# Kernel optimization log

Measured on AMD Instinct MI355X. Metric: run time of the kernel, lower is better.

## Reference

```python
import jax, jax.numpy as jnp
import numpy as np

N, D, E, H, K = 16384, 1024, 16, 4096, 2


def setup_inputs() -> dict:
    key = jax.random.key(0)
    ks = jax.random.split(key, 6)
    s = 0.02
    return {
        "x": jax.random.normal(ks[0], (N, D), jnp.float32),
        "Wr": jax.random.normal(ks[1], (D, E), jnp.float32) * s,
        "br": jnp.zeros((E,), jnp.float32),
        "Wn": jax.random.normal(ks[2], (D, E), jnp.float32) * s,
        "bn": jnp.zeros((E,), jnp.float32),
        "W1": jax.random.normal(ks[3], (E, D, H), jnp.float32) * s,
        "b1": jnp.zeros((E, H), jnp.float32),
        "W2": jax.random.normal(ks[4], (E, H, 1), jnp.float32) * s,
        "b2": jnp.zeros((E, 1), jnp.float32),
        "k": K,
    }


def reference(x, Wr, br, Wn, bn, W1, b1, W2, b2, k):
    # Router. NOTE: faithful to source — top-k and scattered values come from
    # noise_logits; logits/noise feed only noisy_logits which is dead (only used
    # as a shape template for the -inf tensor), so the randn noise is omitted.
    noise_logits = x @ Wn + bn                      # [N, E]
    vals, idx = jax.lax.top_k(noise_logits, k)      # [N, k]
    # softmax over sparse(-inf filled) logits == softmax over top-k values,
    # scattered back; non-selected experts get exactly 0.
    probs = jax.nn.softmax(vals, axis=-1)           # [N, k]
    n = x.shape[0]
    gates = jnp.zeros((n, noise_logits.shape[-1]), x.dtype)
    gates = gates.at[jnp.arange(n)[:, None], idx].set(probs)  # [N, E]

    # Dense loop over ALL experts (as in source), masked-weighted sum.
    def step(acc, per_expert):
        w1, bb1, w2, bb2, g = per_expert
        h = jax.nn.relu(x @ w1 + bb1)               # [N, H]
        out = h @ w2 + bb2                          # [N, 1]
        return acc + out * g[:, None], None

    init = jnp.zeros((n, 1), x.dtype)
    final_out, _ = jax.lax.scan(step, init, (W1, b1, W2, b2, gates.T))
    return final_out
```

## Files before the change

### kernel.cpp

```cpp
#include <hip/hip_runtime.h>
#include <stdint.h>

#define N_TOK 16384
#define DIM   1024
#define NEXP  16
#define HID   4096

typedef unsigned short ushort_t;
typedef __bf16 bf16x8 __attribute__((ext_vector_type(8)));
typedef float  f32x4  __attribute__((ext_vector_type(4)));

__device__ __forceinline__ ushort_t f2bf(float f) {
    union { float f; unsigned int u; } v; v.f = f;
    unsigned int r = v.u + 0x7fffu + ((v.u >> 16) & 1u);
    return (ushort_t)(r >> 16);
}

__device__ __forceinline__ void gl_lds16(const void* g, void* l) {
    __builtin_amdgcn_global_load_lds(
        (const __attribute__((address_space(1))) void*)g,
        (__attribute__((address_space(3))) void*)l, 16, 0, 0);
}

__global__ void __launch_bounds__(256) transpose_w1_kernel(const float* __restrict__ W1,
                                                           ushort_t* __restrict__ w1t) {
    __shared__ float tile[32][33];
    int e  = blockIdx.z;
    int h0 = blockIdx.x * 32;
    int d0 = blockIdx.y * 32;
    const float* src = W1 + (size_t)e * DIM * HID;
#pragma unroll
    for (int j = 0; j < 4; ++j) {
        int d = d0 + threadIdx.y + j * 8;
        tile[threadIdx.y + j * 8][threadIdx.x] = src[(size_t)d * HID + h0 + threadIdx.x];
    }
    __syncthreads();
    ushort_t* dst = w1t + (size_t)e * HID * DIM;
#pragma unroll
    for (int j = 0; j < 4; ++j) {
        int h = h0 + threadIdx.y + j * 8;
        dst[(size_t)h * DIM + d0 + threadIdx.x] = f2bf(tile[threadIdx.x][threadIdx.y + j * 8]);
    }
}

__global__ void __launch_bounds__(256) router_logits_kernel(
    const float* __restrict__ x, const float* __restrict__ Wn,
    const float* __restrict__ bn, const float* __restrict__ b2,
    ushort_t* __restrict__ xbf, int2* __restrict__ eidx,
    float2* __restrict__ probs, float* __restrict__ out) {
    int wave  = threadIdx.x >> 6;
    int lane  = threadIdx.x & 63;
    int token = blockIdx.x * 4 + wave;
    const float* xr = x + (size_t)token * DIM;
    float acc[NEXP];
#pragma unroll
    for (int e = 0; e < NEXP; ++e) acc[e] = 0.f;
    ushort_t xl[16];
#pragma unroll
    for (int i = 0; i < 16; ++i) {
        int d = lane + i * 64;
        float xv = xr[d];
        xl[i] = f2bf(xv);
        const float4* wr = (const float4*)(Wn + d * NEXP);
        float4 w0 = wr[0], w1 = wr[1], w2 = wr[2], w3 = wr[3];
        acc[0]  += xv * w0.x; acc[1]  += xv * w0.y; acc[2]  += xv * w0.z; acc[3]  += xv * w0.w;
        acc[4]  += xv * w1.x; acc[5]  += xv * w1.y; acc[6]  += xv * w1.z; acc[7]  += xv * w1.w;
        acc[8]  += xv * w2.x; acc[9]  += xv * w2.y; acc[10] += xv * w2.z; acc[11] += xv * w2.w;
        acc[12] += xv * w3.x; acc[13] += xv * w3.y; acc[14] += xv * w3.z; acc[15] += xv * w3.w;
    }
    ushort_t* xbr = xbf + (size_t)token * DIM;
#pragma unroll
    for (int i = 0; i < 16; ++i) xbr[lane + i * 64] = xl[i];
#pragma unroll
    for (int e = 0; e < NEXP; ++e) {
        float v = acc[e];
#pragma unroll
        for (int off = 32; off > 0; off >>= 1) v += __shfl_xor(v, off, 64);
        acc[e] = v + bn[e];
    }
    if (lane == 0) {
        float m0 = -1e30f; int i0 = 0;
        for (int e = 0; e < NEXP; ++e) if (acc[e] > m0) { m0 = acc[e]; i0 = e; }
        float m1 = -1e30f; int i1 = 0;
        for (int e = 0; e < NEXP; ++e) if (e != i0 && acc[e] > m1) { m1 = acc[e]; i1 = e; }
        float tq = expf(m1 - m0);
        float p0 = 1.f / (1.f + tq);
        float p1 = 1.f - p0;
        eidx[token]  = make_int2(i0, i1);
        probs[token] = make_float2(p0, p1);
        out[token]   = p0 * b2[i0] + p1 * b2[i1];
    }
}

__global__ void __launch_bounds__(256) bucket_kernel(
    const int2* __restrict__ eidx, const float2* __restrict__ probs,
    int* __restrict__ tok, float* __restrict__ gate, int* __restrict__ cnt) {
    const int e = blockIdx.x;
    const int t = threadIdx.x;
    const int wv = t >> 6, lane = t & 63;
    __shared__ int wsum[4];
    __shared__ int sbase;
    if (t == 0) sbase = 0;
    __syncthreads();
    for (int t0 = 0; t0 < N_TOK; t0 += 256) {
        int token = t0 + t;
        int2  ei = eidx[token];
        float2 pr = probs[token];
        bool sel0 = (ei.x == e);
        bool sel  = sel0 | (ei.y == e);
        float p   = sel0 ? pr.x : pr.y;
        unsigned long long mask = __ballot(sel);
        int wprefix = __popcll(mask & ((1ull << lane) - 1ull));
        if (lane == 0) wsum[wv] = __popcll(mask);
        __syncthreads();
        int off = sbase + wprefix;
        for (int w = 0; w < wv; ++w) off += wsum[w];
        if (sel) {
            tok[e * N_TOK + off]  = token;
            gate[e * N_TOK + off] = p;
        }
        __syncthreads();
        if (t == 0) sbase += wsum[0] + wsum[1] + wsum[2] + wsum[3];
    }
    __syncthreads();
    if (t == 0) cnt[e] = sbase;
}

__global__ void __launch_bounds__(256, 2) moe_ffn_kernel(
    const ushort_t* __restrict__ xbf, const ushort_t* __restrict__ w1t,
    const float* __restrict__ b1, const float* __restrict__ w2,
    const int* __restrict__ tok, const float* __restrict__ gate,
    const int* __restrict__ cnt, float* __restrict__ out) {
    __shared__ ushort_t Alds[128 * 64];
    __shared__ ushort_t Blds[128 * 64];
    const int e  = blockIdx.z;
    const int ce = cnt[e];
    const int m0 = blockIdx.y * 128;
    if (m0 >= ce) return;
    const int h0 = blockIdx.x * 128;
    const int t    = threadIdx.x;
    const int wv   = t >> 6;
    const int lane = t & 63;
    const int quad = lane >> 4;
    const int ln   = lane & 15;
    const int wm   = (wv >> 1) * 64;
    const int wn   = (wv & 1) * 64;

    int tkid[4];
#pragma unroll
    for (int i = 0; i < 4; ++i) {
        int f = i * 256 + t;
        int r = f >> 3;
        int rr = (m0 + r < ce) ? (m0 + r) : m0;
        tkid[i] = tok[e * N_TOK + rr];
    }

    f32x4 acc[4][4];
    const f32x4 zero = {0.f, 0.f, 0.f, 0.f};
#pragma unroll
    for (int mi = 0; mi < 4; ++mi)
#pragma unroll
        for (int ni = 0; ni < 4; ++ni) acc[mi][ni] = zero;

    for (int k0 = 0; k0 < DIM; k0 += 64) {
#pragma unroll
        for (int i = 0; i < 4; ++i) {
            int f = i * 256 + t;
            int r = f >> 3, c = f & 7;
            int cs = (c ^ (r & 7)) << 3;
            const ushort_t* ga = xbf + (size_t)tkid[i] * DIM + k0 + cs;
            gl_lds16(ga, &Alds[f * 8]);
            const ushort_t* gb = w1t + ((size_t)e * HID + h0 + r) * DIM + k0 + cs;
            gl_lds16(gb, &Blds[f * 8]);
        }
        __syncthreads();
#pragma unroll
        for (int ks = 0; ks < 2; ++ks) {
            int q = ks * 4 + quad;
            int csw = (q ^ (ln & 7)) << 3;
            bf16x8 af[4], bfr[4];
#pragma unroll
            for (int mi = 0; mi < 4; ++mi)
                af[mi] = *(const bf16x8*)&Alds[(wm + mi * 16 + ln) * 64 + csw];
#pragma unroll
            for (int ni = 0; ni < 4; ++ni)
                bfr[ni] = *(const bf16x8*)&Blds[(wn + ni * 16 + ln) * 64 + csw];
#pragma unroll
            for (int mi = 0; mi < 4; ++mi)
#pragma unroll
                for (int ni = 0; ni < 4; ++ni)
                    acc[mi][ni] = __builtin_amdgcn_mfma_f32_16x16x32_bf16(
                        af[mi], bfr[ni], acc[mi][ni], 0, 0, 0);
        }
        __syncthreads();
    }

#pragma unroll
    for (int mi = 0; mi < 4; ++mi) {
        float part[4] = {0.f, 0.f, 0.f, 0.f};
#pragma unroll
        for (int ni = 0; ni < 4; ++ni) {
            int h = h0 + wn + ni * 16 + ln;
            float bb = b1[e * HID + h];
            float ww = w2[e * HID + h];
#pragma unroll
            for (int rg = 0; rg < 4; ++rg) {
                float v = acc[mi][ni][rg] + bb;
                v = v > 0.f ? v : 0.f;
                part[rg] += v * ww;
            }
        }
#pragma unroll
        for (int rg = 0; rg < 4; ++rg) {
            float v = part[rg];
            v += __shfl_xor(v, 1, 64);
            v += __shfl_xor(v, 2, 64);
            v += __shfl_xor(v, 4, 64);
            v += __shfl_xor(v, 8, 64);
            part[rg] = v;
        }
        if (ln == 0) {
#pragma unroll
            for (int rg = 0; rg < 4; ++rg) {
                int r = m0 + wm + mi * 16 + quad * 4 + rg;
                if (r < ce) {
                    int tk  = tok[e * N_TOK + r];
                    float g = gate[e * N_TOK + r];
                    atomicAdd(&out[tk], g * part[rg]);
                }
            }
        }
    }
}

extern "C" void kernel_launch(void* const* d_in, const int* in_sizes, int n_in,
                              void* d_out, int out_size, void* d_ws, size_t ws_size,
                              hipStream_t stream) {
    (void)in_sizes; (void)n_in; (void)out_size; (void)ws_size;
    const float* x  = (const float*)d_in[0];
    const float* Wn = (const float*)d_in[3];
    const float* bn = (const float*)d_in[4];
    const float* W1 = (const float*)d_in[5];
    const float* b1 = (const float*)d_in[6];
    const float* W2 = (const float*)d_in[7];
    const float* b2 = (const float*)d_in[8];
    float* out = (float*)d_out;

    char* ws = (char*)d_ws;
    ushort_t* xbf = (ushort_t*)ws;
    ushort_t* w1t = (ushort_t*)(ws + (size_t)32 * 1024 * 1024);
    char* p2 = ws + (size_t)160 * 1024 * 1024;
    int*    tok   = (int*)p2;
    float*  gate  = (float*)(p2 + (size_t)NEXP * N_TOK * 4);
    int*    cnt   = (int*)(p2 + (size_t)2 * NEXP * N_TOK * 4);
    int2*   eidx  = (int2*)(p2 + (size_t)2 * NEXP * N_TOK * 4 + 256);
    float2* probs = (float2*)(p2 + (size_t)2 * NEXP * N_TOK * 4 + 256 + (size_t)N_TOK * 8);

    transpose_w1_kernel<<<dim3(HID / 32, DIM / 32, NEXP), dim3(32, 8), 0, stream>>>(W1, w1t);
    router_logits_kernel<<<N_TOK / 4, 256, 0, stream>>>(x, Wn, bn, b2, xbf, eidx, probs, out);
    bucket_kernel<<<NEXP, 256, 0, stream>>>(eidx, probs, tok, gate, cnt);
    moe_ffn_kernel<<<dim3(HID / 128, 64, NEXP), 256, 0, stream>>>(xbf, w1t, b1, W2, tok,
                                                                  gate, cnt, out);
}
```

Measured before the change: 852.0 us.

## Parallelize expert bucketing with histogram-scan-scatter and vectorize W1 transpose

Replaces the serial 16-block bucket kernel, which walks all tokens sequentially per expert, with a three-stage histogram, prefix-scan and scatter across 64 chunks, so token bucketing runs in parallel. The W1 transpose now uses 64x64 tiles with float4 loads, converts to bf16 before writing to shared memory, and stores 16-byte vectors, cutting memory instructions for the 256MB weight read. This adds two extra kernel launches and keeps the stable per-expert token order.

```diff
diff --git a/kernel.cpp b/kernel.cpp
--- a/kernel.cpp
+++ b/kernel.cpp
@@ -9,6 +9,7 @@
 typedef unsigned short ushort_t;
 typedef __bf16 bf16x8 __attribute__((ext_vector_type(8)));
 typedef float  f32x4  __attribute__((ext_vector_type(4)));
+typedef ushort_t u16x8 __attribute__((ext_vector_type(8)));
 
 __device__ __forceinline__ ushort_t f2bf(float f) {
     union { float f; unsigned int u; } v; v.f = f;
@@ -22,24 +23,36 @@
         (__attribute__((address_space(3))) void*)l, 16, 0, 0);
 }
 
+#define TS 72
 __global__ void __launch_bounds__(256) transpose_w1_kernel(const float* __restrict__ W1,
                                                            ushort_t* __restrict__ w1t) {
-    __shared__ float tile[32][33];
-    int e  = blockIdx.z;
-    int h0 = blockIdx.x * 32;
-    int d0 = blockIdx.y * 32;
+    __shared__ ushort_t tileT[64 * TS];
+    const int e  = blockIdx.z;
+    const int h0 = blockIdx.x * 64;
+    const int d0 = blockIdx.y * 64;
+    const int t  = threadIdx.x;
+    const int hs = t & 15;
+    const int dg = t >> 4;
     const float* src = W1 + (size_t)e * DIM * HID;
+    float4 rows[4];
+#pragma unroll
+    for (int i = 0; i < 4; ++i)
+        rows[i] = *(const float4*)(src + (size_t)(d0 + dg * 4 + i) * HID + h0 + hs * 4);
 #pragma unroll
     for (int j = 0; j < 4; ++j) {
-        int d = d0 + threadIdx.y + j * 8;
-        tile[threadIdx.y + j * 8][threadIdx.x] = src[(size_t)d * HID + h0 + threadIdx.x];
+        float v0 = (&rows[0].x)[j], v1 = (&rows[1].x)[j];
+        float v2 = (&rows[2].x)[j], v3 = (&rows[3].x)[j];
+        ushort4 col; col.x = f2bf(v0); col.y = f2bf(v1); col.z = f2bf(v2); col.w = f2bf(v3);
+        *(ushort4*)&tileT[(hs * 4 + j) * TS + dg * 4] = col;
     }
     __syncthreads();
     ushort_t* dst = w1t + (size_t)e * HID * DIM;
 #pragma unroll
-    for (int j = 0; j < 4; ++j) {
-        int h = h0 + threadIdx.y + j * 8;
-        dst[(size_t)h * DIM + d0 + threadIdx.x] = f2bf(tile[threadIdx.x][threadIdx.y + j * 8]);
+    for (int p = 0; p < 2; ++p) {
+        int r = p * 32 + (t >> 3);
+        int c = t & 7;
+        u16x8 fr = *(const u16x8*)&tileT[r * TS + c * 8];
+        *(u16x8*)(dst + (size_t)(h0 + r) * DIM + d0 + c * 8) = fr;
     }
 }
 
@@ -92,38 +105,69 @@
     }
 }
 
-__global__ void __launch_bounds__(256) bucket_kernel(
+#define NCHUNK 64
+#define CHUNK  (N_TOK / NCHUNK)
+
+__global__ void __launch_bounds__(256) hist_kernel(const int2* __restrict__ eidx,
+                                                   int* __restrict__ counts) {
+    __shared__ int h[NEXP];
+    const int t = threadIdx.x;
+    if (t < NEXP) h[t] = 0;
+    __syncthreads();
+    int token = blockIdx.x * CHUNK + t;
+    int2 ei = eidx[token];
+    atomicAdd(&h[ei.x], 1);
+    atomicAdd(&h[ei.y], 1);
+    __syncthreads();
+    if (t < NEXP) counts[t * NCHUNK + blockIdx.x] = h[t];
+}
+
+__global__ void __launch_bounds__(1024) scan_kernel(const int* __restrict__ counts,
+                                                    int* __restrict__ offs,
+                                                    int* __restrict__ cnt) {
+    const int w    = threadIdx.x >> 6;
+    const int lane = threadIdx.x & 63;
+    int v = counts[w * NCHUNK + lane];
+    int orig = v;
+#pragma unroll
+    for (int off = 1; off < 64; off <<= 1) {
+        int up = __shfl_up(v, off, 64);
+        if (lane >= off) v += up;
+    }
+    offs[w * NCHUNK + lane] = v - orig;
+    if (lane == 63) cnt[w] = v;
+}
+
+__global__ void __launch_bounds__(256) scatter_kernel(
     const int2* __restrict__ eidx, const float2* __restrict__ probs,
-    int* __restrict__ tok, float* __restrict__ gate, int* __restrict__ cnt) {
-    const int e = blockIdx.x;
+    const int* __restrict__ offs, int* __restrict__ tok, float* __restrict__ gate) {
+    __shared__ int wcnt[4][NEXP];
     const int t = threadIdx.x;
     const int wv = t >> 6, lane = t & 63;
-    __shared__ int wsum[4];
-    __shared__ int sbase;
-    if (t == 0) sbase = 0;
+    const int token = blockIdx.x * CHUNK + t;
+    int2  ei = eidx[token];
+    float2 pr = probs[token];
+    unsigned long long lmask = (1ull << lane) - 1ull;
+#pragma unroll
+    for (int e = 0; e < NEXP; ++e) {
+        bool s = (ei.x == e) | (ei.y == e);
+        unsigned long long m = __ballot(s);
+        if (lane == 0) wcnt[wv][e] = __popcll(m);
+    }
     __syncthreads();
-    for (int t0 = 0; t0 < N_TOK; t0 += 256) {
-        int token = t0 + t;
-        int2  ei = eidx[token];
-        float2 pr = probs[token];
-        bool sel0 = (ei.x == e);
-        bool sel  = sel0 | (ei.y == e);
-        float p   = sel0 ? pr.x : pr.y;
-        unsigned long long mask = __ballot(sel);
-        int wprefix = __popcll(mask & ((1ull << lane) - 1ull));
-        if (lane == 0) wsum[wv] = __popcll(mask);
-        __syncthreads();
-        int off = sbase + wprefix;
-        for (int w = 0; w < wv; ++w) off += wsum[w];
-        if (sel) {
-            tok[e * N_TOK + off]  = token;
-            gate[e * N_TOK + off] = p;
-        }
-        __syncthreads();
-        if (t == 0) sbase += wsum[0] + wsum[1] + wsum[2] + wsum[3];
-    }
-    __syncthreads();
-    if (t == 0) cnt[e] = sbase;
+#pragma unroll
+    for (int e = 0; e < NEXP; ++e) {
+        bool s0 = (ei.x == e);
+        bool s  = s0 | (ei.y == e);
+        unsigned long long m = __ballot(s);
+        int base = offs[e * NCHUNK + blockIdx.x];
+        for (int w = 0; w < wv; ++w) base += wcnt[w][e];
+        int pos = base + __popcll(m & lmask);
+        if (s) {
+            tok[e * N_TOK + pos]  = token;
+            gate[e * N_TOK + pos] = s0 ? pr.x : pr.y;
+        }
+    }
 }
 
 __global__ void __launch_bounds__(256, 2) moe_ffn_kernel(
@@ -250,15 +294,20 @@
     ushort_t* xbf = (ushort_t*)ws;
     ushort_t* w1t = (ushort_t*)(ws + (size_t)32 * 1024 * 1024);
     char* p2 = ws + (size_t)160 * 1024 * 1024;
-    int*    tok   = (int*)p2;
-    float*  gate  = (float*)(p2 + (size_t)NEXP * N_TOK * 4);
-    int*    cnt   = (int*)(p2 + (size_t)2 * NEXP * N_TOK * 4);
-    int2*   eidx  = (int2*)(p2 + (size_t)2 * NEXP * N_TOK * 4 + 256);
-    float2* probs = (float2*)(p2 + (size_t)2 * NEXP * N_TOK * 4 + 256 + (size_t)N_TOK * 8);
-
-    transpose_w1_kernel<<<dim3(HID / 32, DIM / 32, NEXP), dim3(32, 8), 0, stream>>>(W1, w1t);
+    size_t off = 0;
+    int*    tok    = (int*)(p2 + off);    off += (size_t)NEXP * N_TOK * 4;
+    float*  gate   = (float*)(p2 + off);  off += (size_t)NEXP * N_TOK * 4;
+    int*    cnt    = (int*)(p2 + off);    off += 256;
+    int2*   eidx   = (int2*)(p2 + off);   off += (size_t)N_TOK * 8;
+    float2* probs  = (float2*)(p2 + off); off += (size_t)N_TOK * 8;
+    int*    counts = (int*)(p2 + off);    off += NEXP * NCHUNK * 4;
+    int*    offs   = (int*)(p2 + off);    off += NEXP * NCHUNK * 4;
+
     router_logits_kernel<<<N_TOK / 4, 256, 0, stream>>>(x, Wn, bn, b2, xbf, eidx, probs, out);
-    bucket_kernel<<<NEXP, 256, 0, stream>>>(eidx, probs, tok, gate, cnt);
+    hist_kernel<<<NCHUNK, 256, 0, stream>>>(eidx, counts);
+    scan_kernel<<<1, 1024, 0, stream>>>(counts, offs, cnt);
+    scatter_kernel<<<NCHUNK, 256, 0, stream>>>(eidx, probs, offs, tok, gate);
+    transpose_w1_kernel<<<dim3(HID / 64, DIM / 64, NEXP), 256, 0, stream>>>(W1, w1t);
     moe_ffn_kernel<<<dim3(HID / 128, 64, NEXP), 256, 0, stream>>>(xbf, w1t, b1, W2, tok,
                                                                   gate, cnt, out);
 }
```

Measured after the change: 835.3 us. About the same (-2.0%).
